# Optimization experiments

Measured on AMD Instinct MI355X. Metric: run time of the kernel, lower is better.

## Reference

```python
import jax, jax.numpy as jnp
from jax import lax
import numpy as np

TAU = 10.0      # tauSr == tauRef
THR = 1.0       # theta
WIDTH = 1.0     # tauRho (surrogate width)
SCALE = 1.0     # scaleRho (surrogate scale)
DECAY = float(np.exp(-1.0 / TAU))


@jax.custom_vjp
def _heaviside(v):
    # spike = 1[v >= theta]
    return (v >= THR).astype(v.dtype)

def _heaviside_fwd(v):
    return _heaviside(v), v

def _heaviside_bwd(v, g):
    # SLAYER exponential surrogate pdf: scaleRho/tauRho * exp(-|v-theta|/tauRho)
    return (g * (SCALE / WIDTH) * jnp.exp(-jnp.abs(v - THR) / WIDTH),)

_heaviside.defvjp(_heaviside_fwd, _heaviside_bwd)


def _conv2d(x, w, pad):
    # x: (B, Cin, H, W), w: (Cout, Cin, kh, kw); SLAYER convs have no bias
    return lax.conv_general_dilated(
        x, w, window_strides=(1, 1), padding=[(pad, pad), (pad, pad)],
        dimension_numbers=("NCHW", "OIHW", "NCHW"))


def _sumpool(x, k):
    # SLAYER pool = sum over kxk window (times a learned scalar applied outside)
    B, C, H, W = x.shape
    return x.reshape(B, C, H // k, k, W // k, k).sum(axis=(3, 5))


def _psp(seq):
    # exponential synaptic (PSP) filter along time: s[t] = a*s[t-1] + x[t]
    a = jnp.asarray(DECAY, seq.dtype)
    def step(s, x_t):
        s = a * s + x_t
        return s, s
    _, out = lax.scan(step, jnp.zeros_like(seq[0]), seq)
    return out  # (T, ...)


def _spikes(u):
    # thresholded spiking with decaying refractory feedback (scaleRef=1):
    # v[t] = u[t] - r[t]; s[t] = 1[v >= theta]; r[t+1] = b*(r[t] + theta*s[t])
    b = jnp.asarray(DECAY, u.dtype)
    def step(r, u_t):
        s = _heaviside(u_t - r)
        r_next = b * (r + THR * s)
        return r_next, s
    _, out = lax.scan(step, jnp.zeros_like(u[0]), u)
    return out  # (T, ...)


def _forward(x, conv1_w, conv2_w, lin_w, w_pool1, w_pool2):
    N, T, C, H, W = x.shape  # (64, 100, 2, 32, 32)
    h = _conv2d(x.reshape(N * T, C, H, W), conv1_w, 2)        # (NT, 4, 32, 32)
    h = _sumpool(h, 4) * w_pool1                               # (NT, 4, 8, 8)
    h = h.reshape(N, T, 4, 8, 8).swapaxes(0, 1)                # (T, N, 4, 8, 8)
    s1 = _spikes(_psp(h))                                      # (T, N, 4, 8, 8)
    h2 = _conv2d(s1.reshape(T * N, 4, 8, 8), conv2_w, 1)       # (TN, 8, 8, 8)
    h2 = (_sumpool(h2, 2) * w_pool2).reshape(T, N, 8, 4, 4)    # (T, N, 8, 4, 4)
    s2 = _spikes(_psp(h2))                                     # (T, N, 8, 4, 4)
    # dense = full-spatial conv (2, 8, 4, 4) -> (N, T, 2)
    return jnp.einsum("tnchw,ochw->nto", s2, lin_w)


def setup_inputs() -> dict:
    key = jax.random.key(0)
    ks = jax.random.split(key, 4)
    x = (jax.random.uniform(ks[0], (64, 100, 2, 32, 32)) < 0.1).astype(jnp.float32)
    conv1_w = jax.random.normal(ks[1], (4, 2, 5, 5), jnp.float32) * 0.3
    conv2_w = jax.random.normal(ks[2], (8, 4, 3, 3), jnp.float32) * 0.3
    lin_w = jax.random.normal(ks[3], (2, 8, 4, 4), jnp.float32) * 0.3
    w_pool1 = jnp.float32(1.0 / 16.0)  # 1.1*theta / (16 * 1.1)
    w_pool2 = jnp.float32(1.0 / 4.0)   # 1.1*theta / (4 * 1.1)
    return {"x": x, "conv1_w": conv1_w, "conv2_w": conv2_w, "lin_w": lin_w,
            "w_pool1": w_pool1, "w_pool2": w_pool2}


def reference(x, conv1_w, conv2_w, lin_w, w_pool1, w_pool2):
    return _forward(x, conv1_w, conv2_w, lin_w, w_pool1, w_pool2)
```

## Files before the change

kernel.cpp:

```cpp
#include <hip/hip_runtime.h>


#define DECAY 0.9048374180359595f

#define BAR_LGKM() asm volatile("s_waitcnt lgkmcnt(0)\n\ts_barrier" ::: "memory")
#define FENCE_LGKM() asm volatile("s_waitcnt lgkmcnt(0)" ::: "memory")

typedef __attribute__((ext_vector_type(8))) _Float16 half8;

__global__ __launch_bounds__(128) void k0_fold(const float* __restrict__ w1,
        const float* __restrict__ wp1, float* __restrict__ wl1) {
    const int idx = blockIdx.x * 128 + threadIdx.x;
    const float p1 = wp1[0];
    const int f = idx & 7, c = (idx >> 3) & 3, e = (idx >> 5) & 7, cin = idx >> 8;
    const int cc = c * 2 + cin;
    int alo = e - 3; if (alo < 0) alo = 0;
    int ahi = e;     if (ahi > 4) ahi = 4;
    int blo = f - 3; if (blo < 0) blo = 0;
    int bhi = f;     if (bhi > 4) bhi = 4;
    float s = 0.f;
    for (int a = alo; a <= ahi; ++a)
        for (int b = blo; b <= bhi; ++b)
            s += w1[cc * 25 + a * 5 + b];
    wl1[(cin * 8 + e) * 32 + c * 8 + f] = s * p1;
}

__global__ __launch_bounds__(64) void k1(const float* __restrict__ x,
        const float* __restrict__ wg, float* __restrict__ u1,
        float* __restrict__ out) {
    __shared__ __align__(16) float xs[2 * 1296];
    __shared__ __align__(16) float wl[512];
    const int lane = threadIdx.x;
    const int frame = blockIdx.x;
    const int n = frame / 100, t = frame % 100;

    if (frame < 50) {
        #pragma unroll
        for (int q = 0; q < 4; ++q)
            out[frame * 256 + q * 64 + lane] = 0.f;
    }

    *(float4*)(wl + 4 * lane)       = *(const float4*)(wg + 4 * lane);
    *(float4*)(wl + 256 + 4 * lane) = *(const float4*)(wg + 256 + 4 * lane);

    #pragma unroll
    for (int m0 = 0; m0 < 128; m0 += 64) {
        const int m = m0 + lane;
        if (m < 72) {
            const int cin = m / 36, rem = m % 36;
            const int rr = rem / 9, q4 = rem % 9;
            const int pr = (rr == 0) ? 0 : (rr == 1) ? 9 : (rr == 2) ? 26 : 35;
            *(float4*)(xs + cin * 1296 + pr * 36 + q4 * 4) = make_float4(0.f, 0.f, 0.f, 0.f);
        }
    }
    #pragma unroll
    for (int m0 = 0; m0 < 192; m0 += 64) {
        const int m = m0 + lane;
        if (m < 144) {
            const int cin = m / 72, rem = m % 72;
            const int side = rem & 1, pr = rem >> 1;
            *(float2*)(xs + cin * 1296 + pr * 36 + side * 34) = make_float2(0.f, 0.f);
        }
    }
    const float4* xg = (const float4*)(x + (size_t)frame * 2048);
    #pragma unroll
    for (int q = 0; q < 8; ++q) {
        const int m = q * 64 + lane;
        const float4 v = xg[m];
        const int li = 4 * m;
        const int cin = li >> 10, row = (li >> 5) & 31, col = li & 31;
        const int r = row + 2;
        const int pr = (r & 3) * 9 + (r >> 2);
        float* d = xs + cin * 1296 + pr * 36 + col + 2;
        *(float2*)(d)     = make_float2(v.x, v.y);
        *(float2*)(d + 2) = make_float2(v.z, v.w);
    }
    FENCE_LGKM();

    const int cp = lane >> 5;
    const int i  = (lane >> 2) & 7;
    const int jh = (lane >> 1) & 1;
    const int eh = lane & 1;

    float acc[2][4] = {{0.f, 0.f, 0.f, 0.f}, {0.f, 0.f, 0.f, 0.f}};
    const float* tb = xs + (i + eh) * 36 + jh * 16;
    #pragma unroll
    for (int cin = 0; cin < 2; ++cin) {
        #pragma unroll
        for (int et = 0; et < 4; ++et) {
            const int ro = cin * 1296 + et * 9 * 36;
            float xr[20];
            #pragma unroll
            for (int b = 0; b < 5; ++b)
                *(float4*)(xr + 4 * b) = *(const float4*)(tb + ro + 4 * b);
            float wv[16];
            const float* wp = wl + (cin * 8 + eh * 4 + et) * 32 + cp * 16;
            #pragma unroll
            for (int q = 0; q < 4; ++q)
                *(float4*)(wv + 4 * q) = *(const float4*)(wp + 4 * q);
            #pragma unroll
            for (int cl = 0; cl < 2; ++cl) {
                #pragma unroll
                for (int jj = 0; jj < 4; ++jj) {
                    const int o = 4 * jj;
                    acc[cl][jj] += xr[o]*wv[cl*8]     + xr[o+1]*wv[cl*8+1]
                                 + xr[o+2]*wv[cl*8+2] + xr[o+3]*wv[cl*8+3]
                                 + xr[o+4]*wv[cl*8+4] + xr[o+5]*wv[cl*8+5]
                                 + xr[o+6]*wv[cl*8+6] + xr[o+7]*wv[cl*8+7];
                }
            }
        }
    }
    #pragma unroll
    for (int cl = 0; cl < 2; ++cl)
        #pragma unroll
        for (int jj = 0; jj < 4; ++jj)
            acc[cl][jj] += __shfl_xor(acc[cl][jj], 1);

    const float o0 = eh ? acc[1][0] : acc[0][0];
    const float o1 = eh ? acc[1][1] : acc[0][1];
    const float o2 = eh ? acc[1][2] : acc[0][2];
    const float o3 = eh ? acc[1][3] : acc[0][3];
    *(float4*)(u1 + (size_t)n * 25600 + t * 256 + (2 * cp + eh) * 64 + i * 8 + jh * 4) =
        make_float4(o0, o1, o2, o3);
}

__global__ __launch_bounds__(256) void k_s(const float* __restrict__ u1,
        _Float16* __restrict__ s1g) {
    const int n = blockIdx.x, tid = threadIdx.x;
    const float a = DECAY;
    const float* up = u1 + (size_t)n * 25600 + tid;
    _Float16* sp = s1g + (size_t)n * 26400 + tid;

    float v[100];
    #pragma unroll
    for (int k = 0; k < 100; ++k) v[k] = up[k * 256];

    float psp = 0.f, rr = 0.f;
    #pragma unroll
    for (int k = 0; k < 100; ++k) {
        psp = a * psp + v[k];
        const float vv = psp - rr;
        const float s = (vv >= 1.f) ? 1.f : 0.f;
        rr = a * (rr + s);
        sp[k * 264] = (_Float16)s;
    }
}

__global__ __launch_bounds__(256, 2) void kf(const _Float16* __restrict__ s1g,
        const float* __restrict__ w2, const float* __restrict__ wp2,
        const float* __restrict__ lw, float* __restrict__ out) {
    __shared__ __align__(16) _Float16 ls1h[100 * 264];
    __shared__ __align__(16) float    ls2[100 * 20 + 64];
    const int tid = threadIdx.x;
    const int bid = blockIdx.x;
    const int n   = (bid & 7) * 8 + (bid >> 6);
    const int oct = (bid >> 3) & 7;
    const int wave = tid >> 6;
    const float a = DECAY;

    const float4* gs = (const float4*)(s1g + (size_t)n * 26400);
    float4 st[13];
    #pragma unroll
    for (int j = 0; j < 13; ++j) {
        const int idx = j * 256 + tid;
        if (idx < 3300) st[j] = gs[idx];
    }

    if (tid < 64) {
        const float p2 = wp2[0];
        const int cin = tid >> 4, e = (tid >> 2) & 3, f = tid & 3;
        int alo = e - 1; if (alo < 0) alo = 0;
        int ahi = e;     if (ahi > 2) ahi = 2;
        int blo = f - 1; if (blo < 0) blo = 0;
        int bhi = f;     if (bhi > 2) bhi = 2;
        float s = 0.f;
        for (int aa = alo; aa <= ahi; ++aa)
            for (int bb = blo; bb <= bhi; ++bb)
                s += w2[((oct * 4 + cin) * 3 + aa) * 3 + bb];
        ls2[2000 + cin * 16 + e * 4 + f] = s * p2;
    }

    #pragma unroll
    for (int j = 0; j < 13; ++j) {
        const int idx = j * 256 + tid;
        if (idx < 3300) *(float4*)((char*)ls1h + idx * 16) = st[j];
    }
    BAR_LGKM();

    float4 wreg[16];
    #pragma unroll
    for (int q = 0; q < 16; ++q)
        wreg[q] = *(const float4*)(ls2 + 2000 + (q >> 2) * 16 + (q & 3) * 4);

    const int sub = tid >> 3, l8 = tid & 7;
    const int i2 = l8 >> 1, jhp = l8 & 1;

    #pragma unroll 1
    for (int pass = 0; pass < 4; ++pass) {
        const int slot = sub + 32 * pass;
        if (slot < 100) {
            const _Float16* sb = ls1h + slot * 264;
            float acc0 = 0.f, acc1 = 0.f;
            #pragma unroll
            for (int cin = 0; cin < 4; ++cin) {
                #pragma unroll
                for (int e = 0; e < 4; ++e) {
                    const int ri = 2 * i2 + e - 1;
                    const int rc = (ri < 0) ? 0 : (ri > 7 ? 7 : ri);
                    const bool rok = (ri >= 0) && (ri <= 7);
                    const half8 hv = *(const half8*)(sb + cin * 64 + rc * 8);
                    float rr8[8];
                    #pragma unroll
                    for (int m = 0; m < 8; ++m) rr8[m] = (float)hv[m];
                    float xr[6];
                    xr[0] = jhp ? rr8[3] : 0.0f;
                    xr[1] = jhp ? rr8[4] : rr8[0];
                    xr[2] = jhp ? rr8[5] : rr8[1];
                    xr[3] = jhp ? rr8[6] : rr8[2];
                    xr[4] = jhp ? rr8[7] : rr8[3];
                    xr[5] = jhp ? 0.0f   : rr8[4];
                    if (!rok) {
                        #pragma unroll
                        for (int m = 0; m < 6; ++m) xr[m] = 0.0f;
                    }
                    const float4 wf = wreg[cin * 4 + e];
                    acc0 += xr[0] * wf.x; acc0 += xr[1] * wf.y;
                    acc0 += xr[2] * wf.z; acc0 += xr[3] * wf.w;
                    acc1 += xr[2] * wf.x; acc1 += xr[3] * wf.y;
                    acc1 += xr[4] * wf.z; acc1 += xr[5] * wf.w;
                }
            }
            *(float2*)(ls2 + slot * 20 + i2 * 4 + 2 * jhp) =
                make_float2(acc0, acc1);
        }
    }
    BAR_LGKM();

    if (wave == 0 && (tid & 63) < 16) {
        const int cell = tid & 63;
        float ub[100];
        #pragma unroll
        for (int k = 0; k < 100; ++k) ub[k] = ls2[k * 20 + cell];
        float psp2 = 0.f, rr2 = 0.f;
        #pragma unroll
        for (int k = 0; k < 100; ++k) {
            psp2 = a * psp2 + ub[k];
            const float vv = psp2 - rr2;
            const float s = (vv >= 1.f) ? 1.f : 0.f;
            rr2 = a * (rr2 + s);
            ls2[k * 20 + cell] = s;
        }
    }
    BAR_LGKM();

    if (tid < 200) {
        const int t = tid >> 1, o = tid & 1;
        const float* srow = ls2 + t * 20;
        const float* wrow = lw + o * 128 + oct * 16;
        const float4 s0 = *(const float4*)(srow);
        const float4 s1 = *(const float4*)(srow + 4);
        const float4 s2 = *(const float4*)(srow + 8);
        const float4 s3 = *(const float4*)(srow + 12);
        const float4 w0 = *(const float4*)(wrow);
        const float4 w1v = *(const float4*)(wrow + 4);
        const float4 w2v = *(const float4*)(wrow + 8);
        const float4 w3 = *(const float4*)(wrow + 12);
        float v = 0.f;
        v += s0.x * w0.x;  v += s0.y * w0.y;  v += s0.z * w0.z;  v += s0.w * w0.w;
        v += s1.x * w1v.x; v += s1.y * w1v.y; v += s1.z * w1v.z; v += s1.w * w1v.w;
        v += s2.x * w2v.x; v += s2.y * w2v.y; v += s2.z * w2v.z; v += s2.w * w2v.w;
        v += s3.x * w3.x;  v += s3.y * w3.y;  v += s3.z * w3.z;  v += s3.w * w3.w;
        atomicAdd(&out[n * 200 + t * 2 + o], v);
    }
}

extern "C" void kernel_launch(void* const* d_in, const int* in_sizes, int n_in,
                              void* d_out, int out_size, void* d_ws, size_t ws_size,
                              hipStream_t stream) {
    const float* x   = (const float*)d_in[0];
    const float* w1  = (const float*)d_in[1];
    const float* w2  = (const float*)d_in[2];
    const float* lw  = (const float*)d_in[3];
    const float* wp1 = (const float*)d_in[4];
    const float* wp2 = (const float*)d_in[5];

    float*     u1  = (float*)d_ws;
    float*     wl1 = u1 + 1638400;
    _Float16*  s1g = (_Float16*)(wl1 + 512);
    float*     out = (float*)d_out;

    k0_fold<<<4, 128, 0, stream>>>(w1, wp1, wl1);
    k1<<<6400, 64, 0, stream>>>(x, wl1, u1, out);
    k_s<<<64, 256, 0, stream>>>(u1, s1g);
    kf<<<512, 256, 0, stream>>>(s1g, w2, wp2, lw, out);
}
```

Measured before the change: 126.9 us.

## Fuse layer-1 PSP/spike scan into final kernel, recomputing per block

Removes the separate spike-generation kernel and its fp16 intermediate buffer. Each final-stage block now reads the layer-1 potentials directly, runs the PSP and refractory scan with a 10-deep rolling prefetch, and writes the spikes straight into shared memory. This saves a launch and a global round trip, and spreads the serial scan over more blocks. The cost is that the scan and the u1 reads are repeated for each of the 8 output-channel groups per sample.

```diff
diff --git a/kernel.cpp b/kernel.cpp
--- a/kernel.cpp
+++ b/kernel.cpp
@@ -125,29 +125,7 @@
         make_float4(o0, o1, o2, o3);
 }
 
-__global__ __launch_bounds__(256) void k_s(const float* __restrict__ u1,
-        _Float16* __restrict__ s1g) {
-    const int n = blockIdx.x, tid = threadIdx.x;
-    const float a = DECAY;
-    const float* up = u1 + (size_t)n * 25600 + tid;
-    _Float16* sp = s1g + (size_t)n * 26400 + tid;
-
-    float v[100];
-    #pragma unroll
-    for (int k = 0; k < 100; ++k) v[k] = up[k * 256];
-
-    float psp = 0.f, rr = 0.f;
-    #pragma unroll
-    for (int k = 0; k < 100; ++k) {
-        psp = a * psp + v[k];
-        const float vv = psp - rr;
-        const float s = (vv >= 1.f) ? 1.f : 0.f;
-        rr = a * (rr + s);
-        sp[k * 264] = (_Float16)s;
-    }
-}
-
-__global__ __launch_bounds__(256, 2) void kf(const _Float16* __restrict__ s1g,
+__global__ __launch_bounds__(256, 2) void kf(const float* __restrict__ u1,
         const float* __restrict__ w2, const float* __restrict__ wp2,
         const float* __restrict__ lw, float* __restrict__ out) {
     __shared__ __align__(16) _Float16 ls1h[100 * 264];
@@ -158,14 +136,6 @@
     const int oct = (bid >> 3) & 7;
     const int wave = tid >> 6;
     const float a = DECAY;
-
-    const float4* gs = (const float4*)(s1g + (size_t)n * 26400);
-    float4 st[13];
-    #pragma unroll
-    for (int j = 0; j < 13; ++j) {
-        const int idx = j * 256 + tid;
-        if (idx < 3300) st[j] = gs[idx];
-    }
 
     if (tid < 64) {
         const float p2 = wp2[0];
@@ -181,10 +151,22 @@
         ls2[2000 + cin * 16 + e * 4 + f] = s * p2;
     }
 
-    #pragma unroll
-    for (int j = 0; j < 13; ++j) {
-        const int idx = j * 256 + tid;
-        if (idx < 3300) *(float4*)((char*)ls1h + idx * 16) = st[j];
+    {
+        const float* up = u1 + (size_t)n * 25600 + tid;
+        float pb[10];
+        #pragma unroll
+        for (int j = 0; j < 10; ++j) pb[j] = up[j * 256];
+        float psp = 0.f, rr = 0.f;
+        #pragma unroll 10
+        for (int k = 0; k < 100; ++k) {
+            const float cur = pb[k % 10];
+            if (k + 10 < 100) pb[k % 10] = up[(k + 10) * 256];
+            psp = a * psp + cur;
+            const float vv = psp - rr;
+            const float s = (vv >= 1.f) ? 1.f : 0.f;
+            rr = a * (rr + s);
+            ls1h[k * 264 + tid] = (_Float16)s;
+        }
     }
     BAR_LGKM();
 
@@ -285,13 +267,11 @@
     const float* wp1 = (const float*)d_in[4];
     const float* wp2 = (const float*)d_in[5];
 
-    float*     u1  = (float*)d_ws;
-    float*     wl1 = u1 + 1638400;
-    _Float16*  s1g = (_Float16*)(wl1 + 512);
-    float*     out = (float*)d_out;
+    float* u1  = (float*)d_ws;
+    float* wl1 = u1 + 1638400;
+    float* out = (float*)d_out;
 
     k0_fold<<<4, 128, 0, stream>>>(w1, wp1, wl1);
     k1<<<6400, 64, 0, stream>>>(x, wl1, u1, out);
-    k_s<<<64, 256, 0, stream>>>(u1, s1g);
-    kf<<<512, 256, 0, stream>>>(s1g, w2, wp2, lw, out);
-}
+    kf<<<512, 256, 0, stream>>>(u1, w2, wp2, lw, out);
+}
```

Measured after the change: 126.1 us. No clear change (-0.6%).
